# Performance work log

Hardware: AMD Instinct MI355X
Metric: run time of the kernel (lower is better)

Reference implementation:

```python
import jax, jax.numpy as jnp
import numpy as np

N = 100000
E = 1600000
IN_DIM, HID_DIM, OUT_DIM = 128, 64, 32
HEADS = 8
NEG_SLOPE = 0.2
NEG_INF = -1e9


def _glorot(key, shape):
    stdv = np.sqrt(6.0 / (shape[-2] + shape[-1]))
    return jax.random.uniform(key, shape, jnp.float32, -stdv, stdv)


def gat_conv(x, src, dst, self_mask, W, att, bias, heads, out_ch, concat):
    """One GATConv layer (eval mode: dropout off). src/dst already include self-loops;
    self_mask marks original edges that were self-loops (removed via -inf score)."""
    n = x.shape[0]
    h = (x @ W).reshape(n, heads, out_ch)              # [N,H,C]
    x_i = h[dst]                                        # [Etot,H,C] gather target
    x_j = h[src]                                        # [Etot,H,C] gather source
    a = jnp.einsum('ehc,hc->eh', x_i, att[0, :, :out_ch]) \
        + jnp.einsum('ehc,hc->eh', x_j, att[0, :, out_ch:])
    alpha = jax.nn.leaky_relu(a, NEG_SLOPE)             # [Etot,H]
    alpha = jnp.where(self_mask[:, None], NEG_INF, alpha)
    amax = jax.lax.stop_gradient(
        jax.ops.segment_max(alpha, dst, num_segments=n))
    ex = jnp.exp(alpha - amax[dst])
    denom = jax.ops.segment_sum(ex, dst, num_segments=n)
    w = ex / denom[dst]                                 # segment softmax over incoming edges
    out = jax.ops.segment_sum(x_j * w[:, :, None], dst, num_segments=n)  # [N,H,C]
    out = out.reshape(n, heads * out_ch) if concat else out.mean(axis=1)
    return out + bias


def setup_inputs() -> dict:
    key = jax.random.key(0)
    ks = jax.random.split(key, 12)
    x = jax.random.normal(ks[0], (N, IN_DIM), jnp.float32)
    edge_index = jax.random.randint(ks[1], (2, E), 0, N, jnp.int64)
    c1 = HID_DIM // HEADS  # 8
    params = {
        'W1': _glorot(ks[2], (IN_DIM, HEADS * c1)),
        'att1': _glorot(ks[3], (1, HEADS, 2 * c1)),
        'b1': jnp.zeros((HID_DIM,), jnp.float32),
        'W2': _glorot(ks[4], (HID_DIM, HEADS * c1)),
        'att2': _glorot(ks[5], (1, HEADS, 2 * c1)),
        'b2': jnp.zeros((HID_DIM,), jnp.float32),
        'W3': _glorot(ks[6], (HID_DIM, 1 * OUT_DIM)),
        'att3': _glorot(ks[7], (1, 1, 2 * OUT_DIM)),
        'b3': jnp.zeros((OUT_DIM,), jnp.float32),
    }
    return dict(x=x, edge_index=edge_index, **params)


def reference(x, edge_index, W1, att1, b1, W2, att2, b2, W3, att3, b3):
    n = x.shape[0]
    src, dst = edge_index[0], edge_index[1]
    loop = jnp.arange(n, dtype=src.dtype)
    src_f = jnp.concatenate([src, loop])
    dst_f = jnp.concatenate([dst, loop])
    # remove_self_loops + add_self_loops: mask original self-loops, append fresh ones
    self_mask = jnp.concatenate([src == dst, jnp.zeros((n,), bool)])
    c1 = HID_DIM // HEADS
    h = jax.nn.elu(gat_conv(x, src_f, dst_f, self_mask, W1, att1, b1, HEADS, c1, True))
    h = jax.nn.elu(gat_conv(h, src_f, dst_f, self_mask, W2, att2, b2, HEADS, c1, True))
    out = gat_conv(h, src_f, dst_f, self_mask, W3, att3, b3, 1, OUT_DIM, False)
    return out
```

## Files before the change

### kernel.cpp

```cpp
#include <hip/hip_runtime.h>
#include <hip/hip_bf16.h>

#define NN 100000
#define EE 1600000

constexpr int SCAN_BLK = 1024;
constexpr int NB_SCAN  = (NN + SCAN_BLK - 1) / SCAN_BLK;

constexpr int NR2 = 8;
constexpr int RSZ = NN / NR2;
constexpr int CH  = 32;
constexpr int CSZ = EE / CH;


__global__ __launch_bounds__(256) void histL_k(const int* __restrict__ ei,
                                               int* __restrict__ CntG) {
    __shared__ int cnt[RSZ];
    int r = blockIdx.x % NR2, c = blockIdx.x / NR2;
    int lo = r * RSZ;
    for (int t = threadIdx.x; t < RSZ; t += 256) cnt[t] = 0;
    __syncthreads();
    const int* __restrict__ dstp = ei + EE;
    int base = c * CSZ;
    int tid = threadIdx.x;
    for (int ii = 0; ii < CSZ; ii += 1024) {
        int off = ii + tid * 4;
        if (off < CSZ) {
            int4 s4 = *(const int4*)&ei[base + off];
            int4 d4 = *(const int4*)&dstp[base + off];
            int dl;
            dl = d4.x - lo; if (dl >= 0 && dl < RSZ && s4.x != d4.x) atomicAdd(&cnt[dl], 1);
            dl = d4.y - lo; if (dl >= 0 && dl < RSZ && s4.y != d4.y) atomicAdd(&cnt[dl], 1);
            dl = d4.z - lo; if (dl >= 0 && dl < RSZ && s4.z != d4.z) atomicAdd(&cnt[dl], 1);
            dl = d4.w - lo; if (dl >= 0 && dl < RSZ && s4.w != d4.w) atomicAdd(&cnt[dl], 1);
        }
    }
    __syncthreads();
    for (int t = threadIdx.x; t < RSZ; t += 256)
        CntG[(size_t)c * NN + lo + t] = cnt[t];
}

__global__ __launch_bounds__(256) void combine_sum_k(int* __restrict__ CntG,
                                                     int* __restrict__ deg,
                                                     int* __restrict__ partials) {
    __shared__ int sh[256];
    int t = threadIdx.x;
    int s_tot = 0;
    #pragma unroll
    for (int k = 0; k < 4; ++k) {
        int d = blockIdx.x * SCAN_BLK + k * 256 + t;
        int run = 0;
        if (d < NN) {
            #pragma unroll 8
            for (int c = 0; c < CH; ++c) {
                int v = CntG[(size_t)c * NN + d];
                CntG[(size_t)c * NN + d] = run;
                run += v;
            }
            deg[d] = run;
        }
        s_tot += run;
    }
    sh[t] = s_tot; __syncthreads();
    for (int off = 128; off > 0; off >>= 1) {
        if (t < off) sh[t] += sh[t + off];
        __syncthreads();
    }
    if (t == 0) partials[blockIdx.x] = sh[0];
}

__global__ void scan_final(const int* __restrict__ deg, const int* __restrict__ partials,
                           int* __restrict__ rowptr) {
    __shared__ int sh[256];
    __shared__ int sp[128];
    int t = threadIdx.x;
    if (t < 128) sp[t] = (t < NB_SCAN) ? partials[t] : 0;
    __syncthreads();
    for (int off = 1; off < 128; off <<= 1) {
        int tmp = 0;
        if (t < 128 && t >= off) tmp = sp[t - off];
        __syncthreads();
        if (t < 128) sp[t] += tmp;
        __syncthreads();
    }
    int pref0 = sp[blockIdx.x] - partials[blockIdx.x];

    int base = blockIdx.x * SCAN_BLK + t * 4;
    int v[4]; int s = 0;
    #pragma unroll
    for (int k = 0; k < 4; ++k) { int i = base + k; v[k] = (i < NN) ? deg[i] : 0; s += v[k]; }
    sh[t] = s; __syncthreads();
    for (int off = 1; off < 256; off <<= 1) {
        int tmp = (t >= off) ? sh[t - off] : 0;
        __syncthreads();
        sh[t] += tmp;
        __syncthreads();
    }
    int pref = pref0 + sh[t] - s;
    #pragma unroll
    for (int k = 0; k < 4; ++k) {
        int i = base + k;
        if (i < NN) {
            rowptr[i] = pref; pref += v[k];
            if (i == NN - 1) rowptr[NN] = pref;
        }
    }
}

__global__ __launch_bounds__(256) void scatterL_k(const int* __restrict__ ei,
                                                  const int* __restrict__ CntG,
                                                  const int* __restrict__ rowptr,
                                                  int* __restrict__ col) {
    __shared__ int cur[RSZ];
    int r = blockIdx.x % NR2, c = blockIdx.x / NR2;
    int lo = r * RSZ;
    for (int t = threadIdx.x; t < RSZ; t += 256)
        cur[t] = rowptr[lo + t] + CntG[(size_t)c * NN + lo + t];
    __syncthreads();
    const int* __restrict__ dstp = ei + EE;
    int base = c * CSZ;
    int tid = threadIdx.x;
    for (int ii = 0; ii < CSZ; ii += 1024) {
        int off = ii + tid * 4;
        if (off < CSZ) {
            int4 s4 = *(const int4*)&ei[base + off];
            int4 d4 = *(const int4*)&dstp[base + off];
            int dl;
            dl = d4.x - lo; if (dl >= 0 && dl < RSZ && s4.x != d4.x) { int p = atomicAdd(&cur[dl], 1); col[p] = s4.x; }
            dl = d4.y - lo; if (dl >= 0 && dl < RSZ && s4.y != d4.y) { int p = atomicAdd(&cur[dl], 1); col[p] = s4.y; }
            dl = d4.z - lo; if (dl >= 0 && dl < RSZ && s4.z != d4.z) { int p = atomicAdd(&cur[dl], 1); col[p] = s4.z; }
            dl = d4.w - lo; if (dl >= 0 && dl < RSZ && s4.w != d4.w) { int p = atomicAdd(&cur[dl], 1); col[p] = s4.w; }
        }
    }
}


template<int K, int M, int H, int NPB>
__global__ __launch_bounds__(256) void gemm_tile(const float* __restrict__ xin,
                          const float* __restrict__ W,
                          const float* __restrict__ att,
                          uint2* __restrict__ Hbf,
                          float* __restrict__ ssrcA,
                          float* __restrict__ sdst) {
    constexpr int C   = M / H;
    constexpr int MG  = M / 4;
    constexpr int NG  = NPB / 4;
    static_assert(MG * NG == 256, "tile mismatch");
    constexpr int K4  = K / 4;
    constexpr int KC4 = (K4 > 16) ? 16 : K4;
    constexpr int NCH = K4 / KC4;

    __shared__ float4 Wq[K * MG];
    __shared__ float4 Xq[NPB * KC4];

    int tid = threadIdx.x;
    const float4* W4 = (const float4*)W;
    for (int i = tid; i < K * MG; i += 256) Wq[i] = W4[i];

    int node0 = blockIdx.x * NPB;
    const float4* x4 = (const float4*)xin;

    int mg = tid % MG, ng = tid / MG;
    int nb = ng * 4;
    float acc[4][4];
    #pragma unroll
    for (int i = 0; i < 4; ++i)
        #pragma unroll
        for (int j = 0; j < 4; ++j) acc[i][j] = 0.f;

    for (int ch = 0; ch < NCH; ++ch) {
        __syncthreads();
        for (int i = tid; i < NPB * KC4; i += 256) {
            int n = i / KC4, k4l = i % KC4;
            int node = node0 + n;
            float4 v = make_float4(0.f, 0.f, 0.f, 0.f);
            if (node < NN) v = x4[(size_t)node * K4 + ch * KC4 + k4l];
            Xq[i] = v;
        }
        __syncthreads();
        #pragma unroll 4
        for (int k4 = 0; k4 < KC4; ++k4) {
            float4 xv[4], wv[4];
            #pragma unroll
            for (int i = 0; i < 4; ++i) xv[i] = Xq[(nb + i) * KC4 + k4];
            int kbase = (ch * KC4 + k4) * 4;
            #pragma unroll
            for (int kk = 0; kk < 4; ++kk) wv[kk] = Wq[(kbase + kk) * MG + mg];
            #pragma unroll
            for (int i = 0; i < 4; ++i) {
                const float* xf = (const float*)&xv[i];
                #pragma unroll
                for (int kk = 0; kk < 4; ++kk) {
                    const float* wf = (const float*)&wv[kk];
                    float xs = xf[kk];
                    acc[i][0] = fmaf(xs, wf[0], acc[i][0]);
                    acc[i][1] = fmaf(xs, wf[1], acc[i][1]);
                    acc[i][2] = fmaf(xs, wf[2], acc[i][2]);
                    acc[i][3] = fmaf(xs, wf[3], acc[i][3]);
                }
            }
        }
    }

    constexpr int TPH = C / 4;
    int head = mg / TPH;
    int c0   = (mg % TPH) * 4;
    float ad[4], as_[4];
    #pragma unroll
    for (int j = 0; j < 4; ++j) {
        ad[j]  = att[head * 2 * C + c0 + j];
        as_[j] = att[head * 2 * C + C + c0 + j];
    }
    #pragma unroll
    for (int i = 0; i < 4; ++i) {
        int node = node0 + nb + i;
        if (node < NN) {
            unsigned short us[4];
            #pragma unroll
            for (int j = 0; j < 4; ++j) {
                __hip_bfloat16 b = __float2bfloat16(acc[i][j]);
                us[j] = *(unsigned short*)&b;
            }
            uint2 pk;
            pk.x = (unsigned)us[0] | ((unsigned)us[1] << 16);
            pk.y = (unsigned)us[2] | ((unsigned)us[3] << 16);
            Hbf[(size_t)node * MG + mg] = pk;
        }
        float pd = acc[i][0]*ad[0]  + acc[i][1]*ad[1]  + acc[i][2]*ad[2]  + acc[i][3]*ad[3];
        float ps = acc[i][0]*as_[0] + acc[i][1]*as_[1] + acc[i][2]*as_[2] + acc[i][3]*as_[3];
        #pragma unroll
        for (int off = 1; off < TPH; off <<= 1) {
            pd += __shfl_xor(pd, off, 64);
            ps += __shfl_xor(ps, off, 64);
        }
        if ((mg % TPH) == 0 && node < NN) {
            sdst[node * H + head]  = pd;
            ssrcA[node * H + head] = ps;
        }
    }
}


template<int CT, int H, int U, bool ELU_OUT>
__global__ __launch_bounds__(256) void agg_k(const int* __restrict__ rowptr, const int* __restrict__ col,
                      const float* __restrict__ sdst, const float* __restrict__ ssrcA,
                      const uint2* __restrict__ Hbf,
                      const float* __restrict__ bias, float* __restrict__ output) {
    constexpr int C    = CT / H;
    constexpr int CP   = CT / 4;
    constexpr int G    = 64 / CP;
    constexpr int NL   = U / G;
    constexpr int EPEL = (U * H >= 64) ? (U * H) / 64 : 1;
    static_assert(EPEL == 1 || EPEL == 2, "mapping");

    int lane = threadIdx.x & 63;
    int node = blockIdx.x * (blockDim.x >> 6) + (threadIdx.x >> 6);
    if (node >= NN) return;

    int cp = lane % CP;
    int pp = lane / CP;
    int hh = (4 * cp) / C;
    int eh = lane % H;
    int gb = lane / H;
    bool elane = (lane < U * H);

    float sd = elane ? sdst[node * H + eh] : 0.f;

    int start = rowptr[node], end = rowptr[node + 1];

    float dsum = 0.f;
    float e_self = 0.f;
    if (lane < H) {
        float ss = ssrcA[node * H + lane];
        float a = sd + ss; a = (a >= 0.f) ? a : 0.2f * a;
        e_self = __expf(a);
        dsum = e_self;
    }
    uint2 hs = Hbf[(size_t)node * CP + cp];
    float exs = __shfl(e_self, hh, 64);
    float4 acc = make_float4(0.f, 0.f, 0.f, 0.f);
    if (pp == 0) {
        acc.x = exs * __uint_as_float(hs.x << 16);
        acc.y = exs * __uint_as_float(hs.x & 0xffff0000u);
        acc.z = exs * __uint_as_float(hs.y << 16);
        acc.w = exs * __uint_as_float(hs.y & 0xffff0000u);
    }

    int cv = node;
    if (start < end) {
        int idx = start + lane;
        if (lane < U && idx < end) cv = col[idx];
    }

    for (int j = start; j < end; j += U) {
        float s1 = 0.f, s2 = 0.f;
        int b1 = 0, b2 = 0;
        if (EPEL == 2) {
            b1 = __shfl(cv, gb, 64);
            b2 = __shfl(cv, gb + U / 2, 64);
            s1 = ssrcA[b1 * H + eh];
            s2 = ssrcA[b2 * H + eh];
        } else {
            b1 = __shfl(cv, gb, 64);
            if (elane) s1 = ssrcA[b1 * H + eh];
        }

        uint2 hv[NL];
        #pragma unroll
        for (int t = 0; t < NL; ++t) {
            int se = __shfl(cv, t * G + pp, 64);
            hv[t] = Hbf[(size_t)se * CP + cp];
        }

        int jn = j + U;
        int cvN = node;
        if (jn < end) {
            int idx = jn + lane;
            if (lane < U && idx < end) cvN = col[idx];
        }

        float e1 = 0.f, e2 = 0.f;
        if (EPEL == 2) {
            float a1 = sd + s1; a1 = (a1 >= 0.f) ? a1 : 0.2f * a1;
            float a2 = sd + s2; a2 = (a2 >= 0.f) ? a2 : 0.2f * a2;
            if (j + gb < end)         e1 = __expf(a1);
            if (j + gb + U / 2 < end) e2 = __expf(a2);
            dsum += e1 + e2;
        } else {
            float a1 = sd + s1; a1 = (a1 >= 0.f) ? a1 : 0.2f * a1;
            if (elane && j + gb < end) { e1 = __expf(a1); dsum += e1; }
        }

        #pragma unroll
        for (int t = 0; t < NL; ++t) {
            int eidx = t * G + pp;
            float ex;
            if (EPEL == 2)
                ex = __shfl((t * G + G - 1 < U / 2) ? e1 : e2, (eidx & (U / 2 - 1)) * H + hh, 64);
            else
                ex = __shfl(e1, eidx * H + hh, 64);
            float f0 = __uint_as_float(hv[t].x << 16);
            float f1 = __uint_as_float(hv[t].x & 0xffff0000u);
            float f2 = __uint_as_float(hv[t].y << 16);
            float f3 = __uint_as_float(hv[t].y & 0xffff0000u);
            acc.x = fmaf(ex, f0, acc.x);
            acc.y = fmaf(ex, f1, acc.y);
            acc.z = fmaf(ex, f2, acc.z);
            acc.w = fmaf(ex, f3, acc.w);
        }
        cv = cvN;
    }

    #pragma unroll
    for (int off = H; off < 64; off <<= 1) dsum += __shfl_xor(dsum, off, 64);
    float den = __shfl(dsum, hh, 64);
    #pragma unroll
    for (int off = CP; off < 64; off <<= 1) {
        acc.x += __shfl_xor(acc.x, off, 64);
        acc.y += __shfl_xor(acc.y, off, 64);
        acc.z += __shfl_xor(acc.z, off, 64);
        acc.w += __shfl_xor(acc.w, off, 64);
    }
    if (lane < CP) {
        float inv = 1.f / den;
        float4 bv = ((const float4*)bias)[cp];
        float4 v;
        v.x = acc.x * inv + bv.x;
        v.y = acc.y * inv + bv.y;
        v.z = acc.z * inv + bv.z;
        v.w = acc.w * inv + bv.w;
        if (ELU_OUT) {
            v.x = (v.x > 0.f) ? v.x : expm1f(v.x);
            v.y = (v.y > 0.f) ? v.y : expm1f(v.y);
            v.z = (v.z > 0.f) ? v.z : expm1f(v.z);
            v.w = (v.w > 0.f) ? v.w : expm1f(v.w);
        }
        ((float4*)output)[(size_t)node * CP + cp] = v;
    }
}


extern "C" void kernel_launch(void* const* d_in, const int* in_sizes, int n_in,
                              void* d_out, int out_size, void* d_ws, size_t ws_size,
                              hipStream_t stream) {
    const float* x    = (const float*)d_in[0];
    const int*   ei   = (const int*)d_in[1];
    const float* W1   = (const float*)d_in[2];
    const float* att1 = (const float*)d_in[3];
    const float* b1   = (const float*)d_in[4];
    const float* W2   = (const float*)d_in[5];
    const float* att2 = (const float*)d_in[6];
    const float* b2   = (const float*)d_in[7];
    const float* W3   = (const float*)d_in[8];
    const float* att3 = (const float*)d_in[9];
    const float* b3   = (const float*)d_in[10];
    float* out = (float*)d_out;

    char* p = (char*)d_ws;
    auto alloc = [&](size_t bytes) -> void* {
        void* r = (void*)p;
        p += (bytes + 255) & ~(size_t)255;
        return r;
    };
    int*   rowptr   = (int*)alloc((NN + 1) * sizeof(int));
    int*   deg      = (int*)alloc(NN * sizeof(int));
    int*   CntG     = (int*)alloc((size_t)CH * NN * sizeof(int));
    int*   partials = (int*)alloc(NB_SCAN * sizeof(int));
    int*   col      = (int*)alloc(EE * sizeof(int));
    float* sdst     = (float*)alloc((size_t)NN * 8 * sizeof(float));
    float* ssrcA    = (float*)alloc((size_t)NN * 8 * sizeof(float));
    uint2* Hbf      = (uint2*)alloc((size_t)NN * 16 * sizeof(uint2));
    float* Fb       = (float*)alloc((size_t)NN * 64 * sizeof(float));

    histL_k<<<CH * NR2, 256, 0, stream>>>(ei, CntG);
    combine_sum_k<<<NB_SCAN, 256, 0, stream>>>(CntG, deg, partials);
    scan_final<<<NB_SCAN, 256, 0, stream>>>(deg, partials, rowptr);
    scatterL_k<<<CH * NR2, 256, 0, stream>>>(ei, CntG, rowptr, col);

    gemm_tile<128, 64, 8, 64><<<(NN + 63) / 64, 256, 0, stream>>>(x, W1, att1, Hbf, ssrcA, sdst);
    agg_k<64, 8, 16, true><<<(NN + 3) / 4, 256, 0, stream>>>(rowptr, col, sdst, ssrcA, Hbf, b1, Fb);

    gemm_tile<64, 64, 8, 64><<<(NN + 63) / 64, 256, 0, stream>>>(Fb, W2, att2, Hbf, ssrcA, sdst);
    agg_k<64, 8, 16, true><<<(NN + 3) / 4, 256, 0, stream>>>(rowptr, col, sdst, ssrcA, Hbf, b2, Fb);

    gemm_tile<64, 32, 1, 128><<<(NN + 127) / 128, 256, 0, stream>>>(Fb, W3, att3, Hbf, ssrcA, sdst);
    agg_k<32, 1, 32, false><<<(NN + 3) / 4, 256, 0, stream>>>(rowptr, col, sdst, ssrcA, Hbf, b3, out);
}
```

Measured before the change: 410.6 us.

## Fuse next-layer GEMM into aggregation and merge CSR scatter with layer-1 GEMM

The CSR scatter kernel and the first-layer GEMM now run as one launch, with blocks split by index, so the independent work can overlap. The layer-2 and layer-3 GEMMs plus their attention-score projections are folded into the tail of the preceding aggregation kernel: each wavefront multiplies its ELU output by the next weight matrix through shuffles and writes bf16 features and scores directly. This removes the fp32 intermediate feature buffer round-trip and two GEMM launches. In exchange, each wave reads the weights per node from global/L1 instead of shared tiles and does a serial shuffle-based matvec, and the combined launch relies on the scan having finished before the GEMM blocks, which stream ordering already guarantees.

```diff
diff --git a/kernel.cpp b/kernel.cpp
--- a/kernel.cpp
+++ b/kernel.cpp
@@ -11,6 +11,7 @@
 constexpr int RSZ = NN / NR2;
 constexpr int CH  = 32;
 constexpr int CSZ = EE / CH;
+constexpr int SCAT_B = CH * NR2;
 
 
 __global__ __launch_bounds__(256) void histL_k(const int* __restrict__ ei,
@@ -107,57 +108,58 @@
     }
 }
 
-__global__ __launch_bounds__(256) void scatterL_k(const int* __restrict__ ei,
-                                                  const int* __restrict__ CntG,
-                                                  const int* __restrict__ rowptr,
-                                                  int* __restrict__ col) {
-    __shared__ int cur[RSZ];
-    int r = blockIdx.x % NR2, c = blockIdx.x / NR2;
-    int lo = r * RSZ;
-    for (int t = threadIdx.x; t < RSZ; t += 256)
-        cur[t] = rowptr[lo + t] + CntG[(size_t)c * NN + lo + t];
-    __syncthreads();
-    const int* __restrict__ dstp = ei + EE;
-    int base = c * CSZ;
+
+__global__ __launch_bounds__(256) void sg1_k(const int* __restrict__ ei,
+                                             const int* __restrict__ CntG,
+                                             const int* __restrict__ rowptr,
+                                             int* __restrict__ col,
+                                             const float* __restrict__ xin,
+                                             const float* __restrict__ W,
+                                             const float* __restrict__ att,
+                                             uint2* __restrict__ Hbf,
+                                             float* __restrict__ ssrcA,
+                                             float* __restrict__ sdst) {
+    extern __shared__ char smem[];
     int tid = threadIdx.x;
-    for (int ii = 0; ii < CSZ; ii += 1024) {
-        int off = ii + tid * 4;
-        if (off < CSZ) {
-            int4 s4 = *(const int4*)&ei[base + off];
-            int4 d4 = *(const int4*)&dstp[base + off];
-            int dl;
-            dl = d4.x - lo; if (dl >= 0 && dl < RSZ && s4.x != d4.x) { int p = atomicAdd(&cur[dl], 1); col[p] = s4.x; }
-            dl = d4.y - lo; if (dl >= 0 && dl < RSZ && s4.y != d4.y) { int p = atomicAdd(&cur[dl], 1); col[p] = s4.y; }
-            dl = d4.z - lo; if (dl >= 0 && dl < RSZ && s4.z != d4.z) { int p = atomicAdd(&cur[dl], 1); col[p] = s4.z; }
-            dl = d4.w - lo; if (dl >= 0 && dl < RSZ && s4.w != d4.w) { int p = atomicAdd(&cur[dl], 1); col[p] = s4.w; }
-        }
-    }
-}
-
-
-template<int K, int M, int H, int NPB>
-__global__ __launch_bounds__(256) void gemm_tile(const float* __restrict__ xin,
-                          const float* __restrict__ W,
-                          const float* __restrict__ att,
-                          uint2* __restrict__ Hbf,
-                          float* __restrict__ ssrcA,
-                          float* __restrict__ sdst) {
-    constexpr int C   = M / H;
+
+    if (blockIdx.x < SCAT_B) {
+        int* cur = (int*)smem;
+        int r = blockIdx.x % NR2, c = blockIdx.x / NR2;
+        int lo = r * RSZ;
+        for (int t = tid; t < RSZ; t += 256)
+            cur[t] = rowptr[lo + t] + CntG[(size_t)c * NN + lo + t];
+        __syncthreads();
+        const int* __restrict__ dstp = ei + EE;
+        int base = c * CSZ;
+        for (int ii = 0; ii < CSZ; ii += 1024) {
+            int off = ii + tid * 4;
+            if (off < CSZ) {
+                int4 s4 = *(const int4*)&ei[base + off];
+                int4 d4 = *(const int4*)&dstp[base + off];
+                int dl;
+                dl = d4.x - lo; if (dl >= 0 && dl < RSZ && s4.x != d4.x) { int p = atomicAdd(&cur[dl], 1); col[p] = s4.x; }
+                dl = d4.y - lo; if (dl >= 0 && dl < RSZ && s4.y != d4.y) { int p = atomicAdd(&cur[dl], 1); col[p] = s4.y; }
+                dl = d4.z - lo; if (dl >= 0 && dl < RSZ && s4.z != d4.z) { int p = atomicAdd(&cur[dl], 1); col[p] = s4.z; }
+                dl = d4.w - lo; if (dl >= 0 && dl < RSZ && s4.w != d4.w) { int p = atomicAdd(&cur[dl], 1); col[p] = s4.w; }
+            }
+        }
+        return;
+    }
+
+    constexpr int K = 128, M = 64, Hh = 8, NPB = 64;
+    constexpr int C   = M / Hh;
     constexpr int MG  = M / 4;
-    constexpr int NG  = NPB / 4;
-    static_assert(MG * NG == 256, "tile mismatch");
     constexpr int K4  = K / 4;
-    constexpr int KC4 = (K4 > 16) ? 16 : K4;
+    constexpr int KC4 = 16;
     constexpr int NCH = K4 / KC4;
 
-    __shared__ float4 Wq[K * MG];
-    __shared__ float4 Xq[NPB * KC4];
-
-    int tid = threadIdx.x;
+    float4* Wq = (float4*)smem;
+    float4* Xq = Wq + K * MG;
+
     const float4* W4 = (const float4*)W;
     for (int i = tid; i < K * MG; i += 256) Wq[i] = W4[i];
 
-    int node0 = blockIdx.x * NPB;
+    int node0 = (blockIdx.x - SCAT_B) * NPB;
     const float4* x4 = (const float4*)xin;
 
     int mg = tid % MG, ng = tid / MG;
@@ -234,24 +236,30 @@
             ps += __shfl_xor(ps, off, 64);
         }
         if ((mg % TPH) == 0 && node < NN) {
-            sdst[node * H + head]  = pd;
-            ssrcA[node * H + head] = ps;
+            sdst[node * Hh + head]  = pd;
+            ssrcA[node * Hh + head] = ps;
         }
     }
 }
 
 
-template<int CT, int H, int U, bool ELU_OUT>
-__global__ __launch_bounds__(256) void agg_k(const int* __restrict__ rowptr, const int* __restrict__ col,
+template<int CT, int H, int U, int NM, int NH>
+__global__ __launch_bounds__(256) void aggF_k(const int* __restrict__ rowptr, const int* __restrict__ col,
                       const float* __restrict__ sdst, const float* __restrict__ ssrcA,
                       const uint2* __restrict__ Hbf,
-                      const float* __restrict__ bias, float* __restrict__ output) {
+                      const float* __restrict__ bias,
+                      const float* __restrict__ Wn,
+                      const float* __restrict__ attn,
+                      unsigned short* __restrict__ Hbf2,
+                      float* __restrict__ ssrcA2,
+                      float* __restrict__ sdst2) {
     constexpr int C    = CT / H;
     constexpr int CP   = CT / 4;
     constexpr int G    = 64 / CP;
     constexpr int NL   = U / G;
     constexpr int EPEL = (U * H >= 64) ? (U * H) / 64 : 1;
     static_assert(EPEL == 1 || EPEL == 2, "mapping");
+    constexpr int NC   = NM / NH;
 
     int lane = threadIdx.x & 63;
     int node = blockIdx.x * (blockDim.x >> 6) + (threadIdx.x >> 6);
@@ -361,6 +369,175 @@
         acc.z += __shfl_xor(acc.z, off, 64);
         acc.w += __shfl_xor(acc.w, off, 64);
     }
+
+    float inv = 1.f / den;
+    float4 bv = ((const float4*)bias)[cp];
+    float4 v;
+    v.x = acc.x * inv + bv.x;
+    v.y = acc.y * inv + bv.y;
+    v.z = acc.z * inv + bv.z;
+    v.w = acc.w * inv + bv.w;
+    v.x = (v.x > 0.f) ? v.x : expm1f(v.x);
+    v.y = (v.y > 0.f) ? v.y : expm1f(v.y);
+    v.z = (v.z > 0.f) ? v.z : expm1f(v.z);
+    v.w = (v.w > 0.f) ? v.w : expm1f(v.w);
+
+    float h2 = 0.f;
+    #pragma unroll
+    for (int q = 0; q < CP; ++q) {
+        float fx = __shfl(v.x, q, 64);
+        float fy = __shfl(v.y, q, 64);
+        float fz = __shfl(v.z, q, 64);
+        float fw = __shfl(v.w, q, 64);
+        if (lane < NM) {
+            h2 = fmaf(fx, Wn[(4 * q + 0) * NM + lane], h2);
+            h2 = fmaf(fy, Wn[(4 * q + 1) * NM + lane], h2);
+            h2 = fmaf(fz, Wn[(4 * q + 2) * NM + lane], h2);
+            h2 = fmaf(fw, Wn[(4 * q + 3) * NM + lane], h2);
+        }
+    }
+
+    int nhead = (lane < NM) ? (lane / NC) : 0;
+    int nc    = lane % NC;
+    float pd = h2 * attn[nhead * 2 * NC + nc];
+    float ps = h2 * attn[nhead * 2 * NC + NC + nc];
+    #pragma unroll
+    for (int off = 1; off < NC; off <<= 1) {
+        pd += __shfl_xor(pd, off, 64);
+        ps += __shfl_xor(ps, off, 64);
+    }
+    if (lane < NM && nc == 0) {
+        sdst2[node * NH + nhead]  = pd;
+        ssrcA2[node * NH + nhead] = ps;
+    }
+
+    if (lane < NM) {
+        __hip_bfloat16 b = __float2bfloat16(h2);
+        Hbf2[(size_t)node * NM + lane] = *(unsigned short*)&b;
+    }
+}
+
+
+template<int CT, int H, int U, bool ELU_OUT>
+__global__ __launch_bounds__(256) void agg_k(const int* __restrict__ rowptr, const int* __restrict__ col,
+                      const float* __restrict__ sdst, const float* __restrict__ ssrcA,
+                      const uint2* __restrict__ Hbf,
+                      const float* __restrict__ bias, float* __restrict__ output) {
+    constexpr int C    = CT / H;
+    constexpr int CP   = CT / 4;
+    constexpr int G    = 64 / CP;
+    constexpr int NL   = U / G;
+    constexpr int EPEL = (U * H >= 64) ? (U * H) / 64 : 1;
+    static_assert(EPEL == 1 || EPEL == 2, "mapping");
+
+    int lane = threadIdx.x & 63;
+    int node = blockIdx.x * (blockDim.x >> 6) + (threadIdx.x >> 6);
+    if (node >= NN) return;
+
+    int cp = lane % CP;
+    int pp = lane / CP;
+    int hh = (4 * cp) / C;
+    int eh = lane % H;
+    int gb = lane / H;
+    bool elane = (lane < U * H);
+
+    float sd = elane ? sdst[node * H + eh] : 0.f;
+
+    int start = rowptr[node], end = rowptr[node + 1];
+
+    float dsum = 0.f;
+    float e_self = 0.f;
+    if (lane < H) {
+        float ss = ssrcA[node * H + lane];
+        float a = sd + ss; a = (a >= 0.f) ? a : 0.2f * a;
+        e_self = __expf(a);
+        dsum = e_self;
+    }
+    uint2 hs = Hbf[(size_t)node * CP + cp];
+    float exs = __shfl(e_self, hh, 64);
+    float4 acc = make_float4(0.f, 0.f, 0.f, 0.f);
+    if (pp == 0) {
+        acc.x = exs * __uint_as_float(hs.x << 16);
+        acc.y = exs * __uint_as_float(hs.x & 0xffff0000u);
+        acc.z = exs * __uint_as_float(hs.y << 16);
+        acc.w = exs * __uint_as_float(hs.y & 0xffff0000u);
+    }
+
+    int cv = node;
+    if (start < end) {
+        int idx = start + lane;
+        if (lane < U && idx < end) cv = col[idx];
+    }
+
+    for (int j = start; j < end; j += U) {
+        float s1 = 0.f, s2 = 0.f;
+        int b1 = 0, b2 = 0;
+        if (EPEL == 2) {
+            b1 = __shfl(cv, gb, 64);
+            b2 = __shfl(cv, gb + U / 2, 64);
+            s1 = ssrcA[b1 * H + eh];
+            s2 = ssrcA[b2 * H + eh];
+        } else {
+            b1 = __shfl(cv, gb, 64);
+            if (elane) s1 = ssrcA[b1 * H + eh];
+        }
+
+        uint2 hv[NL];
+        #pragma unroll
+        for (int t = 0; t < NL; ++t) {
+            int se = __shfl(cv, t * G + pp, 64);
+            hv[t] = Hbf[(size_t)se * CP + cp];
+        }
+
+        int jn = j + U;
+        int cvN = node;
+        if (jn < end) {
+            int idx = jn + lane;
+            if (lane < U && idx < end) cvN = col[idx];
+        }
+
+        float e1 = 0.f, e2 = 0.f;
+        if (EPEL == 2) {
+            float a1 = sd + s1; a1 = (a1 >= 0.f) ? a1 : 0.2f * a1;
+            float a2 = sd + s2; a2 = (a2 >= 0.f) ? a2 : 0.2f * a2;
+            if (j + gb < end)         e1 = __expf(a1);
+            if (j + gb + U / 2 < end) e2 = __expf(a2);
+            dsum += e1 + e2;
+        } else {
+            float a1 = sd + s1; a1 = (a1 >= 0.f) ? a1 : 0.2f * a1;
+            if (elane && j + gb < end) { e1 = __expf(a1); dsum += e1; }
+        }
+
+        #pragma unroll
+        for (int t = 0; t < NL; ++t) {
+            int eidx = t * G + pp;
+            float ex;
+            if (EPEL == 2)
+                ex = __shfl((t * G + G - 1 < U / 2) ? e1 : e2, (eidx & (U / 2 - 1)) * H + hh, 64);
+            else
+                ex = __shfl(e1, eidx * H + hh, 64);
+            float f0 = __uint_as_float(hv[t].x << 16);
+            float f1 = __uint_as_float(hv[t].x & 0xffff0000u);
+            float f2 = __uint_as_float(hv[t].y << 16);
+            float f3 = __uint_as_float(hv[t].y & 0xffff0000u);
+            acc.x = fmaf(ex, f0, acc.x);
+            acc.y = fmaf(ex, f1, acc.y);
+            acc.z = fmaf(ex, f2, acc.z);
+            acc.w = fmaf(ex, f3, acc.w);
+        }
+        cv = cvN;
+    }
+
+    #pragma unroll
+    for (int off = H; off < 64; off <<= 1) dsum += __shfl_xor(dsum, off, 64);
+    float den = __shfl(dsum, hh, 64);
+    #pragma unroll
+    for (int off = CP; off < 64; off <<= 1) {
+        acc.x += __shfl_xor(acc.x, off, 64);
+        acc.y += __shfl_xor(acc.y, off, 64);
+        acc.z += __shfl_xor(acc.z, off, 64);
+        acc.w += __shfl_xor(acc.w, off, 64);
+    }
     if (lane < CP) {
         float inv = 1.f / den;
         float4 bv = ((const float4*)bias)[cp];
@@ -407,22 +584,30 @@
     int*   CntG     = (int*)alloc((size_t)CH * NN * sizeof(int));
     int*   partials = (int*)alloc(NB_SCAN * sizeof(int));
     int*   col      = (int*)alloc(EE * sizeof(int));
-    float* sdst     = (float*)alloc((size_t)NN * 8 * sizeof(float));
-    float* ssrcA    = (float*)alloc((size_t)NN * 8 * sizeof(float));
-    uint2* Hbf      = (uint2*)alloc((size_t)NN * 16 * sizeof(uint2));
-    float* Fb       = (float*)alloc((size_t)NN * 64 * sizeof(float));
+    float* sdst1    = (float*)alloc((size_t)NN * 8 * sizeof(float));
+    float* ssrcA1   = (float*)alloc((size_t)NN * 8 * sizeof(float));
+    uint2* Hbf1     = (uint2*)alloc((size_t)NN * 16 * sizeof(uint2));
+    float* sdst2    = (float*)alloc((size_t)NN * 8 * sizeof(float));
+    float* ssrcA2   = (float*)alloc((size_t)NN * 8 * sizeof(float));
+    unsigned short* Hbf2 = (unsigned short*)alloc((size_t)NN * 64 * sizeof(unsigned short));
+    float* sdst3    = (float*)alloc((size_t)NN * sizeof(float));
+    float* ssrcA3   = (float*)alloc((size_t)NN * sizeof(float));
+    unsigned short* Hbf3 = (unsigned short*)alloc((size_t)NN * 32 * sizeof(unsigned short));
 
     histL_k<<<CH * NR2, 256, 0, stream>>>(ei, CntG);
     combine_sum_k<<<NB_SCAN, 256, 0, stream>>>(CntG, deg, partials);
     scan_final<<<NB_SCAN, 256, 0, stream>>>(deg, partials, rowptr);
-    scatterL_k<<<CH * NR2, 256, 0, stream>>>(ei, CntG, rowptr, col);
-
-    gemm_tile<128, 64, 8, 64><<<(NN + 63) / 64, 256, 0, stream>>>(x, W1, att1, Hbf, ssrcA, sdst);
-    agg_k<64, 8, 16, true><<<(NN + 3) / 4, 256, 0, stream>>>(rowptr, col, sdst, ssrcA, Hbf, b1, Fb);
-
-    gemm_tile<64, 64, 8, 64><<<(NN + 63) / 64, 256, 0, stream>>>(Fb, W2, att2, Hbf, ssrcA, sdst);
-    agg_k<64, 8, 16, true><<<(NN + 3) / 4, 256, 0, stream>>>(rowptr, col, sdst, ssrcA, Hbf, b2, Fb);
-
-    gemm_tile<64, 32, 1, 128><<<(NN + 127) / 128, 256, 0, stream>>>(Fb, W3, att3, Hbf, ssrcA, sdst);
-    agg_k<32, 1, 32, false><<<(NN + 3) / 4, 256, 0, stream>>>(rowptr, col, sdst, ssrcA, Hbf, b3, out);
+
+    constexpr int SMEM = RSZ * (int)sizeof(int);
+    sg1_k<<<SCAT_B + (NN + 63) / 64, 256, SMEM, stream>>>(ei, CntG, rowptr, col,
+                                                          x, W1, att1, Hbf1, ssrcA1, sdst1);
+
+    aggF_k<64, 8, 16, 64, 8><<<(NN + 3) / 4, 256, 0, stream>>>(rowptr, col, sdst1, ssrcA1, Hbf1, b1,
+                                                               W2, att2, Hbf2, ssrcA2, sdst2);
+
+    aggF_k<64, 8, 16, 32, 1><<<(NN + 3) / 4, 256, 0, stream>>>(rowptr, col, sdst2, ssrcA2, (const uint2*)Hbf2, b2,
+                                                               W3, att3, Hbf3, ssrcA3, sdst3);
+
+    agg_k<32, 1, 32, false><<<(NN + 3) / 4, 256, 0, stream>>>(rowptr, col, sdst3, ssrcA3, (const uint2*)Hbf3,
+                                                              b3, out);
 }
```

Result: slower. 462.7 us (+12.7%).

## Fuse edge scatter and first-layer GEMM into one heterogeneous kernel launch

Applied to the files above, without the earlier changes.

Merges the CSR scatter kernel and the layer-1 projection GEMM into a single launch. The first blocks do the scatter and the remaining blocks do the GEMM, so the two independent phases can overlap and one launch disappears. Dynamic shared memory is sized to the scatter's 50KB counter array, which the GEMM blocks reuse for W and X tiles (32KB+4KB). The larger shared allocation applies to all blocks and may lower occupancy for the GEMM blocks.

```diff
diff --git a/kernel.cpp b/kernel.cpp
--- a/kernel.cpp
+++ b/kernel.cpp
@@ -11,6 +11,7 @@
 constexpr int RSZ = NN / NR2;
 constexpr int CH  = 32;
 constexpr int CSZ = EE / CH;
+constexpr int SCAT_B = CH * NR2;
 
 
 __global__ __launch_bounds__(256) void histL_k(const int* __restrict__ ei,
@@ -107,29 +108,136 @@
     }
 }
 
-__global__ __launch_bounds__(256) void scatterL_k(const int* __restrict__ ei,
-                                                  const int* __restrict__ CntG,
-                                                  const int* __restrict__ rowptr,
-                                                  int* __restrict__ col) {
-    __shared__ int cur[RSZ];
-    int r = blockIdx.x % NR2, c = blockIdx.x / NR2;
-    int lo = r * RSZ;
-    for (int t = threadIdx.x; t < RSZ; t += 256)
-        cur[t] = rowptr[lo + t] + CntG[(size_t)c * NN + lo + t];
-    __syncthreads();
-    const int* __restrict__ dstp = ei + EE;
-    int base = c * CSZ;
+
+__global__ __launch_bounds__(256) void sg1_k(const int* __restrict__ ei,
+                                             const int* __restrict__ CntG,
+                                             const int* __restrict__ rowptr,
+                                             int* __restrict__ col,
+                                             const float* __restrict__ xin,
+                                             const float* __restrict__ W,
+                                             const float* __restrict__ att,
+                                             uint2* __restrict__ Hbf,
+                                             float* __restrict__ ssrcA,
+                                             float* __restrict__ sdst) {
+    extern __shared__ char smem[];
     int tid = threadIdx.x;
-    for (int ii = 0; ii < CSZ; ii += 1024) {
-        int off = ii + tid * 4;
-        if (off < CSZ) {
-            int4 s4 = *(const int4*)&ei[base + off];
-            int4 d4 = *(const int4*)&dstp[base + off];
-            int dl;
-            dl = d4.x - lo; if (dl >= 0 && dl < RSZ && s4.x != d4.x) { int p = atomicAdd(&cur[dl], 1); col[p] = s4.x; }
-            dl = d4.y - lo; if (dl >= 0 && dl < RSZ && s4.y != d4.y) { int p = atomicAdd(&cur[dl], 1); col[p] = s4.y; }
-            dl = d4.z - lo; if (dl >= 0 && dl < RSZ && s4.z != d4.z) { int p = atomicAdd(&cur[dl], 1); col[p] = s4.z; }
-            dl = d4.w - lo; if (dl >= 0 && dl < RSZ && s4.w != d4.w) { int p = atomicAdd(&cur[dl], 1); col[p] = s4.w; }
+
+    if (blockIdx.x < SCAT_B) {
+        int* cur = (int*)smem;
+        int r = blockIdx.x % NR2, c = blockIdx.x / NR2;
+        int lo = r * RSZ;
+        for (int t = tid; t < RSZ; t += 256)
+            cur[t] = rowptr[lo + t] + CntG[(size_t)c * NN + lo + t];
+        __syncthreads();
+        const int* __restrict__ dstp = ei + EE;
+        int base = c * CSZ;
+        for (int ii = 0; ii < CSZ; ii += 1024) {
+            int off = ii + tid * 4;
+            if (off < CSZ) {
+                int4 s4 = *(const int4*)&ei[base + off];
+                int4 d4 = *(const int4*)&dstp[base + off];
+                int dl;
+                dl = d4.x - lo; if (dl >= 0 && dl < RSZ && s4.x != d4.x) { int p = atomicAdd(&cur[dl], 1); col[p] = s4.x; }
+                dl = d4.y - lo; if (dl >= 0 && dl < RSZ && s4.y != d4.y) { int p = atomicAdd(&cur[dl], 1); col[p] = s4.y; }
+                dl = d4.z - lo; if (dl >= 0 && dl < RSZ && s4.z != d4.z) { int p = atomicAdd(&cur[dl], 1); col[p] = s4.z; }
+                dl = d4.w - lo; if (dl >= 0 && dl < RSZ && s4.w != d4.w) { int p = atomicAdd(&cur[dl], 1); col[p] = s4.w; }
+            }
+        }
+        return;
+    }
+
+    constexpr int K = 128, M = 64, Hh = 8, NPB = 64;
+    constexpr int C   = M / Hh;
+    constexpr int MG  = M / 4;
+    constexpr int K4  = K / 4;
+    constexpr int KC4 = 16;
+    constexpr int NCH = K4 / KC4;
+
+    float4* Wq = (float4*)smem;
+    float4* Xq = Wq + K * MG;
+
+    const float4* W4 = (const float4*)W;
+    for (int i = tid; i < K * MG; i += 256) Wq[i] = W4[i];
+
+    int node0 = (blockIdx.x - SCAT_B) * NPB;
+    const float4* x4 = (const float4*)xin;
+
+    int mg = tid % MG, ng = tid / MG;
+    int nb = ng * 4;
+    float acc[4][4];
+    #pragma unroll
+    for (int i = 0; i < 4; ++i)
+        #pragma unroll
+        for (int j = 0; j < 4; ++j) acc[i][j] = 0.f;
+
+    for (int ch = 0; ch < NCH; ++ch) {
+        __syncthreads();
+        for (int i = tid; i < NPB * KC4; i += 256) {
+            int n = i / KC4, k4l = i % KC4;
+            int node = node0 + n;
+            float4 v = make_float4(0.f, 0.f, 0.f, 0.f);
+            if (node < NN) v = x4[(size_t)node * K4 + ch * KC4 + k4l];
+            Xq[i] = v;
+        }
+        __syncthreads();
+        #pragma unroll 4
+        for (int k4 = 0; k4 < KC4; ++k4) {
+            float4 xv[4], wv[4];
+            #pragma unroll
+            for (int i = 0; i < 4; ++i) xv[i] = Xq[(nb + i) * KC4 + k4];
+            int kbase = (ch * KC4 + k4) * 4;
+            #pragma unroll
+            for (int kk = 0; kk < 4; ++kk) wv[kk] = Wq[(kbase + kk) * MG + mg];
+            #pragma unroll
+            for (int i = 0; i < 4; ++i) {
+                const float* xf = (const float*)&xv[i];
+                #pragma unroll
+                for (int kk = 0; kk < 4; ++kk) {
+                    const float* wf = (const float*)&wv[kk];
+                    float xs = xf[kk];
+                    acc[i][0] = fmaf(xs, wf[0], acc[i][0]);
+                    acc[i][1] = fmaf(xs, wf[1], acc[i][1]);
+                    acc[i][2] = fmaf(xs, wf[2], acc[i][2]);
+                    acc[i][3] = fmaf(xs, wf[3], acc[i][3]);
+                }
+            }
+        }
+    }
+
+    constexpr int TPH = C / 4;
+    int head = mg / TPH;
+    int c0   = (mg % TPH) * 4;
+    float ad[4], as_[4];
+    #pragma unroll
+    for (int j = 0; j < 4; ++j) {
+        ad[j]  = att[head * 2 * C + c0 + j];
+        as_[j] = att[head * 2 * C + C + c0 + j];
+    }
+    #pragma unroll
+    for (int i = 0; i < 4; ++i) {
+        int node = node0 + nb + i;
+        if (node < NN) {
+            unsigned short us[4];
+            #pragma unroll
+            for (int j = 0; j < 4; ++j) {
+                __hip_bfloat16 b = __float2bfloat16(acc[i][j]);
+                us[j] = *(unsigned short*)&b;
+            }
+            uint2 pk;
+            pk.x = (unsigned)us[0] | ((unsigned)us[1] << 16);
+            pk.y = (unsigned)us[2] | ((unsigned)us[3] << 16);
+            Hbf[(size_t)node * MG + mg] = pk;
+        }
+        float pd = acc[i][0]*ad[0]  + acc[i][1]*ad[1]  + acc[i][2]*ad[2]  + acc[i][3]*ad[3];
+        float ps = acc[i][0]*as_[0] + acc[i][1]*as_[1] + acc[i][2]*as_[2] + acc[i][3]*as_[3];
+        #pragma unroll
+        for (int off = 1; off < TPH; off <<= 1) {
+            pd += __shfl_xor(pd, off, 64);
+            ps += __shfl_xor(ps, off, 64);
+        }
+        if ((mg % TPH) == 0 && node < NN) {
+            sdst[node * Hh + head]  = pd;
+            ssrcA[node * Hh + head] = ps;
         }
     }
 }
@@ -415,9 +523,11 @@
     histL_k<<<CH * NR2, 256, 0, stream>>>(ei, CntG);
     combine_sum_k<<<NB_SCAN, 256, 0, stream>>>(CntG, deg, partials);
     scan_final<<<NB_SCAN, 256, 0, stream>>>(deg, partials, rowptr);
-    scatterL_k<<<CH * NR2, 256, 0, stream>>>(ei, CntG, rowptr, col);
-
-    gemm_tile<128, 64, 8, 64><<<(NN + 63) / 64, 256, 0, stream>>>(x, W1, att1, Hbf, ssrcA, sdst);
+
+    constexpr int SMEM = RSZ * (int)sizeof(int);
+    sg1_k<<<SCAT_B + (NN + 63) / 64, 256, SMEM, stream>>>(ei, CntG, rowptr, col,
+                                                          x, W1, att1, Hbf, ssrcA, sdst);
+
     agg_k<64, 8, 16, true><<<(NN + 3) / 4, 256, 0, stream>>>(rowptr, col, sdst, ssrcA, Hbf, b1, Fb);
 
     gemm_tile<64, 64, 8, 64><<<(NN + 63) / 64, 256, 0, stream>>>(Fb, W2, att2, Hbf, ssrcA, sdst);
```

Measured after the change: 385.5 us. 6.1% less time.
